# Performance work log

Measured on AMD Instinct MI355X. Metric: run time of the kernel, lower is better.

Reference implementation:

```python
import jax, jax.numpy as jnp
import numpy as np

N = 10000   # num nodes
E = 320000  # num edges (avg degree 32)
F = 128     # feat_size
H = 128     # hidden_size


def setup_inputs() -> dict:
    key = jax.random.key(0)
    ks = jax.random.split(key, 16)

    def p(k, shape, scale=0.05):
        return jax.random.normal(k, shape, jnp.float32) * scale

    inp = {
        "x": p(ks[0], (N, F), 1.0),
        "edge_index": jax.random.randint(ks[1], (2, E), 0, N),
    }
    # 6 SAGEConv layers: encoder (F->H, H->H), attr decoder (H->H, H->F),
    # struct decoder (H->H, H->N). Each has W_l (neighbor), b_l, W_r (root).
    dims = [(F, H), (H, H), (H, H), (H, F), (H, H), (H, N)]
    names = ["e1", "e2", "a1", "a2", "s1", "s2"]
    i = 2
    for name, (din, dout) in zip(names, dims):
        inp[f"Wl_{name}"] = p(ks[i], (din, dout))
        inp[f"bl_{name}"] = jnp.zeros((dout,), jnp.float32)
        inp[f"Wr_{name}"] = p(ks[i + 1], (din, dout))
        i += 2
    return inp


def sage(x, src, dst, Wl, bl, Wr, n):
    # PyG SAGEConv (aggr='mean'): mean of source-node features at each target,
    # then out = agg @ W_l + b + x @ W_r (root weight).
    msg = jax.ops.segment_sum(x[src], dst, num_segments=n)          # [n, din]
    deg = jax.ops.segment_sum(jnp.ones((src.shape[0],), x.dtype), dst, num_segments=n)
    agg = msg / jnp.maximum(deg, 1.0)[:, None]
    return agg @ Wl + bl + x @ Wr


def reference(x, edge_index,
              Wl_e1, bl_e1, Wr_e1, Wl_e2, bl_e2, Wr_e2,
              Wl_a1, bl_a1, Wr_a1, Wl_a2, bl_a2, Wr_a2,
              Wl_s1, bl_s1, Wr_s1, Wl_s2, bl_s2, Wr_s2):
    src, dst = edge_index[0], edge_index[1]
    n = x.shape[0]
    # Encoder (dropout is identity in eval mode)
    h = jax.nn.relu(sage(x, src, dst, Wl_e1, bl_e1, Wr_e1, n))
    h = jax.nn.relu(sage(h, src, dst, Wl_e2, bl_e2, Wr_e2, n))
    # Attribute decoder -> x_hat [N, F]
    xh = jax.nn.relu(sage(h, src, dst, Wl_a1, bl_a1, Wr_a1, n))
    xh = jax.nn.relu(sage(xh, src, dst, Wl_a2, bl_a2, Wr_a2, n))
    # Structure decoder -> [N, N], transposed as in the original
    s = jax.nn.relu(sage(h, src, dst, Wl_s1, bl_s1, Wr_s1, n))
    s = jax.nn.relu(sage(s, src, dst, Wl_s2, bl_s2, Wr_s2, n)).T
    return (s, xh)
```

## Files before the change

kernel.cpp:

```cpp
#include <hip/hip_runtime.h>
#include <hip/hip_bf16.h>

typedef unsigned short ushort_t;
typedef unsigned int uint_t;
typedef __attribute__((ext_vector_type(8))) short short8;
typedef __attribute__((ext_vector_type(4))) float float4v;

__device__ __forceinline__ float bf2f(ushort_t u) {
    union { uint_t i; float f; } c; c.i = ((uint_t)u) << 16; return c.f;
}
__device__ __forceinline__ ushort_t f2bf(float f) {
    union { float f; uint_t i; } c; c.f = f;
    uint_t x = c.i;
    uint_t r = x + 0x7fffu + ((x >> 16) & 1u);
    return (ushort_t)(r >> 16);
}

__device__ __forceinline__ void gl_lds16(const void* g, void* l) {
    __builtin_amdgcn_global_load_lds(
        (const __attribute__((address_space(1))) void*)g,
        (__attribute__((address_space(3))) void*)l, 16, 0, 0);
}

__device__ __forceinline__ void stv(float* p, float v) { *p = v; }
__device__ __forceinline__ void stv(ushort_t* p, float v) { *p = f2bf(v); }

__global__ void hist_kernel(const int* __restrict__ dstv, int* __restrict__ cnt, int E) {
    int e = blockIdx.x * 256 + threadIdx.x;
    if (e < E) atomicAdd(&cnt[dstv[e]], 1);
}

__global__ __launch_bounds__(1024) void scan_kernel(
    const int* __restrict__ cnt, int* __restrict__ rowptr,
    int* __restrict__ cursor, float* __restrict__ deginv, int n) {
    __shared__ int sums[1024];
    const int t = threadIdx.x;
    const int per = (n + 1023) >> 10;
    const int b0 = t * per;
    int s = 0;
    for (int u = 0; u < per; u++) {
        int i = b0 + u;
        if (i < n) s += cnt[i];
    }
    sums[t] = s;
    __syncthreads();
    int x = s;
    for (int off = 1; off < 1024; off <<= 1) {
        int y = (t >= off) ? sums[t - off] : 0;
        __syncthreads();
        x += y;
        sums[t] = x;
        __syncthreads();
    }
    int run = x - s;
    for (int u = 0; u < per; u++) {
        int i = b0 + u;
        if (i < n) {
            int v = cnt[i];
            rowptr[i] = run;
            cursor[i] = run;
            deginv[i] = 1.0f / (float)(v > 0 ? v : 1);
            run += v;
        }
    }
    if (t == 1023) rowptr[n] = x;
}

__global__ void scatter_kernel(const int* __restrict__ srcv, const int* __restrict__ dstv,
                               int* __restrict__ cursor, int* __restrict__ srcs_sorted, int E) {
    int e = blockIdx.x * 256 + threadIdx.x;
    if (e < E) {
        int p = atomicAdd(&cursor[dstv[e]], 1);
        srcs_sorted[p] = srcv[e];
    }
}

__global__ __launch_bounds__(256) void transpose_w_kernel(
    const float* __restrict__ W0, const float* __restrict__ W1,
    ushort_t* __restrict__ WT, int Nout) {
    __shared__ ushort_t tile[64][72];
    const int i0 = blockIdx.x * 64;
    const int k0 = blockIdx.y * 64;
    const float* W = (k0 < 128) ? (W0 + (size_t)k0 * Nout)
                                : (W1 + (size_t)(k0 - 128) * Nout);
    const int tid = threadIdx.x;
    const int li = tid & 63;
    const int kq = tid >> 6;
    const int gi = i0 + li;
    const bool ok = gi < Nout;
    for (int k = kq; k < 64; k += 4) {
        float v = ok ? W[(size_t)k * Nout + gi] : 0.f;
        tile[li][k] = f2bf(v);
    }
    __syncthreads();
    for (int s = tid; s < 512; s += 256) {
        int r = s >> 3, ch = s & 7;
        int gi2 = i0 + r;
        if (gi2 < Nout)
            *(short8*)(WT + (size_t)gi2 * 256 + k0 + ch * 8) = *(const short8*)&tile[r][ch * 8];
    }
}

struct W5 { const float* W0[5]; const float* W1[5]; };
__global__ __launch_bounds__(256) void transpose_w5_kernel(W5 wp, ushort_t* __restrict__ WT) {
    __shared__ ushort_t tile[64][72];
    const int layer = blockIdx.z;
    const int i0 = blockIdx.x * 64;
    const int k0 = blockIdx.y * 64;
    const float* W = (k0 < 128) ? (wp.W0[layer] + (size_t)k0 * 128)
                                : (wp.W1[layer] + (size_t)(k0 - 128) * 128);
    ushort_t* WTb = WT + (size_t)layer * 128 * 256;
    const int tid = threadIdx.x;
    const int li = tid & 63;
    const int kq = tid >> 6;
    const int gi = i0 + li;
    for (int k = kq; k < 64; k += 4)
        tile[li][k] = f2bf(W[(size_t)k * 128 + gi]);
    __syncthreads();
    for (int s = tid; s < 512; s += 256) {
        int r = s >> 3, ch = s & 7;
        *(short8*)(WTb + (size_t)(i0 + r) * 256 + k0 + ch * 8) = *(const short8*)&tile[r][ch * 8];
    }
}

template <typename TIN>
__device__ __forceinline__ float2 ld2(const TIN* act, size_t row, int t);
template <>
__device__ __forceinline__ float2 ld2<float>(const float* act, size_t row, int t) {
    return ((const float2*)act)[row * 64 + t];
}
template <>
__device__ __forceinline__ float2 ld2<ushort_t>(const ushort_t* act, size_t row, int t) {
    uint_t u = ((const uint_t*)act)[row * 64 + t];
    float2 r; r.x = bf2f((ushort_t)(u & 0xffffu)); r.y = bf2f((ushort_t)(u >> 16));
    return r;
}

template <typename TIN>
__global__ __launch_bounds__(256) void aggregate_kernel(
    const TIN* __restrict__ act, const int* __restrict__ srcs,
    const int* __restrict__ rowptr, const float* __restrict__ deginv,
    ushort_t* __restrict__ Acat, int N) {
    int node = blockIdx.x * 4 + (threadIdx.x >> 6);
    if (node >= N) return;
    int t = threadIdx.x & 63;
    int e0 = rowptr[node], e1 = rowptr[node + 1];
    float ax = 0.f, ay = 0.f;
    int e = e0;
    for (; e + 4 <= e1; e += 4) {
        int s0 = srcs[e], s1 = srcs[e + 1], s2 = srcs[e + 2], s3 = srcs[e + 3];
        float2 v0 = ld2(act, (size_t)s0, t);
        float2 v1 = ld2(act, (size_t)s1, t);
        float2 v2 = ld2(act, (size_t)s2, t);
        float2 v3 = ld2(act, (size_t)s3, t);
        ax += v0.x + v1.x + v2.x + v3.x;
        ay += v0.y + v1.y + v2.y + v3.y;
    }
    for (; e < e1; e++) {
        float2 v = ld2(act, (size_t)srcs[e], t);
        ax += v.x; ay += v.y;
    }
    float dinv = deginv[node];
    uint_t m = ((uint_t)f2bf(ay * dinv) << 16) | (uint_t)f2bf(ax * dinv);
    float2 self = ld2(act, (size_t)node, t);
    uint_t sf = ((uint_t)f2bf(self.y) << 16) | (uint_t)f2bf(self.x);
    ((uint_t*)Acat)[(size_t)node * 128 + t]      = m;
    ((uint_t*)Acat)[(size_t)node * 128 + 64 + t] = sf;
}

__global__ __launch_bounds__(256) void aggregate2_kernel(
    const ushort_t* __restrict__ act, const int* __restrict__ srcs,
    const int* __restrict__ rowptr, const float* __restrict__ deginv,
    ushort_t* __restrict__ AcatA, ushort_t* __restrict__ AcatS, int N) {
    int node = blockIdx.x * 4 + (threadIdx.x >> 6);
    if (node >= N) return;
    int t = threadIdx.x & 63;
    const uint_t* A = (const uint_t*)act;
    int e0 = rowptr[node], e1 = rowptr[node + 1];
    float ax = 0.f, ay = 0.f, sx = 0.f, sy = 0.f;
    int e = e0;
    for (; e + 2 <= e1; e += 2) {
        size_t r0 = (size_t)srcs[e] * 128, r1 = (size_t)srcs[e + 1] * 128;
        uint_t ua0 = A[r0 + t], us0 = A[r0 + 64 + t];
        uint_t ua1 = A[r1 + t], us1 = A[r1 + 64 + t];
        ax += bf2f((ushort_t)(ua0 & 0xffffu)) + bf2f((ushort_t)(ua1 & 0xffffu));
        ay += bf2f((ushort_t)(ua0 >> 16))     + bf2f((ushort_t)(ua1 >> 16));
        sx += bf2f((ushort_t)(us0 & 0xffffu)) + bf2f((ushort_t)(us1 & 0xffffu));
        sy += bf2f((ushort_t)(us0 >> 16))     + bf2f((ushort_t)(us1 >> 16));
    }
    if (e < e1) {
        size_t r0 = (size_t)srcs[e] * 128;
        uint_t ua0 = A[r0 + t], us0 = A[r0 + 64 + t];
        ax += bf2f((ushort_t)(ua0 & 0xffffu));
        ay += bf2f((ushort_t)(ua0 >> 16));
        sx += bf2f((ushort_t)(us0 & 0xffffu));
        sy += bf2f((ushort_t)(us0 >> 16));
    }
    float dinv = deginv[node];
    size_t rb = (size_t)node * 128;
    uint_t sa = A[rb + t], ss = A[rb + 64 + t];
    ((uint_t*)AcatA)[rb + t]      = ((uint_t)f2bf(ay * dinv) << 16) | (uint_t)f2bf(ax * dinv);
    ((uint_t*)AcatA)[rb + 64 + t] = sa;
    ((uint_t*)AcatS)[rb + t]      = ((uint_t)f2bf(sy * dinv) << 16) | (uint_t)f2bf(sx * dinv);
    ((uint_t*)AcatS)[rb + 64 + t] = ss;
}

template <bool BIAS_I, bool SWZ, typename TOUT>
__global__ __launch_bounds__(256) void gemm_nt_kernel(
    const ushort_t* __restrict__ A, const ushort_t* __restrict__ B,
    const float* __restrict__ bias, const float* __restrict__ bias2, int jsplit,
    TOUT* __restrict__ C, int rowsA, int rowsB, int tilesM, int tilesN) {
    __shared__ __align__(16) ushort_t Alds[128 * 64];
    __shared__ __align__(16) ushort_t Blds[128 * 64];

    int pid_m, pid_n;
    if (SWZ) {
        const int lin = blockIdx.x;
        const int nwg = gridDim.x;
        const int w = (lin & 7) * (nwg >> 3) + (lin >> 3);
        const int tM8 = (tilesM + 7) >> 3;
        const int sg = w >> 6, is = w & 63;
        const int sgm = sg % tM8, sgn = sg / tM8;
        pid_m = sgm * 8 + (is & 7);
        pid_n = sgn * 8 + (is >> 3);
        if (pid_m >= tilesM || pid_n >= tilesN) return;
    } else {
        const int lin = blockIdx.x;
        const int GRP = 8;
        const int nig = GRP * tilesN;
        const int gidg = lin / nig;
        const int first_m = gidg * GRP;
        const int gsz = min(tilesM - first_m, GRP);
        const int in_grp = lin - gidg * nig;
        pid_m = first_m + (in_grp % gsz);
        pid_n = in_grp / gsz;
    }
    const int i0 = pid_m * 128;
    const int j0 = pid_n * 128;

    const int tid  = threadIdx.x;
    const int lane = tid & 63;
    const int wid  = tid >> 6;
    const int wm = wid >> 1, wn = wid & 1;
    const int r16 = lane & 15, quad = lane >> 4;
    const int rsub = lane >> 3;
    const int csw  = (lane & 7) ^ rsub;

    float4v acc[4][4];
#pragma unroll
    for (int a = 0; a < 4; a++)
#pragma unroll
        for (int b = 0; b < 4; b++) acc[a][b] = (float4v){0.f, 0.f, 0.f, 0.f};

    for (int kt = 0; kt < 4; kt++) {
        __syncthreads();
        const int kbase = kt * 64 + csw * 8;
#pragma unroll
        for (int t = 0; t < 4; t++) {
            const int w8 = (wid * 4 + t) * 8;
            int rA = min(i0 + w8 + rsub, rowsA - 1);
            gl_lds16(A + (size_t)rA * 256 + kbase, Alds + w8 * 64);
            int rB = min(j0 + w8 + rsub, rowsB - 1);
            gl_lds16(B + (size_t)rB * 256 + kbase, Blds + w8 * 64);
        }
        __syncthreads();
#pragma unroll
        for (int ks = 0; ks < 2; ks++) {
            const int chb = ks * 4 + quad;
            const int sw = ((chb ^ (r16 & 7))) * 8;
            short8 af[4], bfr[4];
#pragma unroll
            for (int im = 0; im < 4; im++)
                af[im] = *(const short8*)(Alds + (wm * 64 + im * 16 + r16) * 64 + sw);
#pragma unroll
            for (int jn = 0; jn < 4; jn++)
                bfr[jn] = *(const short8*)(Blds + (wn * 64 + jn * 16 + r16) * 64 + sw);
#pragma unroll
            for (int im = 0; im < 4; im++)
#pragma unroll
                for (int jn = 0; jn < 4; jn++)
                    acc[im][jn] = __builtin_amdgcn_mfma_f32_16x16x32_bf16(
                        af[im], bfr[jn], acc[im][jn], 0, 0, 0);
        }
    }

    const int rows_lim = rowsA - i0;
    const int cols_lim = rowsB - j0;
#pragma unroll
    for (int im = 0; im < 4; im++) {
#pragma unroll
        for (int jn = 0; jn < 4; jn++) {
            const int jl = wn * 64 + jn * 16 + r16;
            if (jl < cols_lim) {
                float bj = 0.f;
                if (!BIAS_I) {
                    int jg = j0 + jl;
                    bj = (jg >= jsplit) ? bias2[jg - jsplit] : bias[jg];
                }
#pragma unroll
                for (int r = 0; r < 4; r++) {
                    const int il = wm * 64 + im * 16 + quad * 4 + r;
                    if (il < rows_lim) {
                        float bv = BIAS_I ? bias[i0 + il] : bj;
                        float v = fmaxf(acc[im][jn][r] + bv, 0.f);
                        stv(C + (size_t)(i0 + il) * rowsB + (j0 + jl), v);
                    }
                }
            }
        }
    }
}

extern "C" void kernel_launch(void* const* d_in, const int* in_sizes, int n_in,
                              void* d_out, int out_size, void* d_ws, size_t ws_size,
                              hipStream_t stream) {
    const int N = in_sizes[18];
    const int E = in_sizes[1] / 2;

    const float* x = (const float*)d_in[0];
    const int* ei = (const int*)d_in[1];
    const int* srcv = ei;
    const int* dstv = ei + E;

    const float* Wl[6] = {(const float*)d_in[2],  (const float*)d_in[5],
                          (const float*)d_in[8],  (const float*)d_in[11],
                          (const float*)d_in[14], (const float*)d_in[17]};
    const float* bl[6] = {(const float*)d_in[3],  (const float*)d_in[6],
                          (const float*)d_in[9],  (const float*)d_in[12],
                          (const float*)d_in[15], (const float*)d_in[18]};
    const float* Wr[6] = {(const float*)d_in[4],  (const float*)d_in[7],
                          (const float*)d_in[10], (const float*)d_in[13],
                          (const float*)d_in[16], (const float*)d_in[19]};

    char* p = (char*)d_ws;
    auto carve = [&](size_t bytes) -> char* {
        char* q = p;
        p += (bytes + 255) & ~(size_t)255;
        return q;
    };
    int*      cnt    = (int*)carve((size_t)N * 4);
    int*      rowptr = (int*)carve((size_t)(N + 1) * 4);
    int*      cursor = (int*)carve((size_t)N * 4);
    float*    deginv = (float*)carve((size_t)N * 4);
    int*      srcs   = (int*)carve((size_t)E * 4);
    ushort_t* Acat   = (ushort_t*)carve((size_t)N * 256 * 2);
    ushort_t* AcatS  = (ushort_t*)carve((size_t)N * 256 * 2);
    ushort_t* hbA    = (ushort_t*)carve((size_t)N * 128 * 2);
    ushort_t* hbB    = (ushort_t*)carve((size_t)N * 128 * 2);
    ushort_t* hbC    = (ushort_t*)carve((size_t)N * 256 * 2);
    ushort_t* WTs2   = (ushort_t*)carve((size_t)N * 256 * 2);
    ushort_t* WsT    = (ushort_t*)carve((size_t)5 * 128 * 256 * 2);

    hipMemsetAsync(cnt, 0, (size_t)N * 4, stream);
    hist_kernel<<<(E + 255) / 256, 256, 0, stream>>>(dstv, cnt, E);
    scan_kernel<<<1, 1024, 0, stream>>>(cnt, rowptr, cursor, deginv, N);
    scatter_kernel<<<(E + 255) / 256, 256, 0, stream>>>(srcv, dstv, cursor, srcs, E);

    W5 w5;
    w5.W0[0] = Wl[0]; w5.W1[0] = Wr[0];
    w5.W0[1] = Wl[1]; w5.W1[1] = Wr[1];
    w5.W0[2] = Wl[2]; w5.W1[2] = Wr[2];
    w5.W0[3] = Wl[4]; w5.W1[3] = Wr[4];
    w5.W0[4] = Wl[3]; w5.W1[4] = Wr[3];
    transpose_w5_kernel<<<dim3(2, 4, 5), 256, 0, stream>>>(w5, WsT);
    transpose_w_kernel<<<dim3((N + 63) / 64, 4), 256, 0, stream>>>(
        Wl[5], Wr[5], WTs2, N);

    float* outp = (float*)d_out;
    float* xh_out = outp + (size_t)N * N;

    const int tM = (N + 127) / 128;
    const int BIG = 1 << 30;

    aggregate_kernel<float><<<(N + 3) / 4, 256, 0, stream>>>(x, srcs, rowptr, deginv, Acat, N);
    gemm_nt_kernel<false, false, ushort_t><<<tM, 256, 0, stream>>>(
        Acat, WsT + 0 * 128 * 256, bl[0], nullptr, BIG, hbA, N, 128, tM, 1);
    aggregate_kernel<ushort_t><<<(N + 3) / 4, 256, 0, stream>>>(hbA, srcs, rowptr, deginv, Acat, N);
    gemm_nt_kernel<false, false, ushort_t><<<tM, 256, 0, stream>>>(
        Acat, WsT + 1 * 128 * 256, bl[1], nullptr, BIG, hbB, N, 128, tM, 1);
    aggregate_kernel<ushort_t><<<(N + 3) / 4, 256, 0, stream>>>(hbB, srcs, rowptr, deginv, Acat, N);
    gemm_nt_kernel<false, false, ushort_t><<<tM * 2, 256, 0, stream>>>(
        Acat, WsT + 2 * 128 * 256, bl[2], bl[4], 128, hbC, N, 256, tM, 2);
    aggregate2_kernel<<<(N + 3) / 4, 256, 0, stream>>>(hbC, srcs, rowptr, deginv, Acat, AcatS, N);
    gemm_nt_kernel<false, false, float><<<tM, 256, 0, stream>>>(
        Acat, WsT + 4 * 128 * 256, bl[3], nullptr, BIG, xh_out, N, 128, tM, 1);
    const int tM8 = (tM + 7) / 8;
    gemm_nt_kernel<true, true, float><<<tM8 * tM8 * 64, 256, 0, stream>>>(
        WTs2, AcatS, bl[5], nullptr, BIG, outp, N, N, tM, tM);

    (void)n_in; (void)out_size; (void)ws_size;
}
```

Baseline: 750.2 us.

## Stage fp32 GEMM epilogue through LDS for coalesced stores; 64-row tiles for small GEMMs

The fp32 output epilogue now writes each 32-row chunk of the accumulator tile into shared memory and then stores it back as row-contiguous float4 writes. This targets the big N×N structure output, whose per-lane scalar stores were strided. The small 128-wide GEMMs switch to 64-row M tiles to launch more workgroups, and the dual aggregation loop is unrolled by four edges to keep more gathers in flight. The LDS staging adds extra syncthreads per chunk and reuses the operand buffers.

```diff
diff --git a/kernel.cpp b/kernel.cpp
--- a/kernel.cpp
+++ b/kernel.cpp
@@ -179,16 +179,23 @@
     int e0 = rowptr[node], e1 = rowptr[node + 1];
     float ax = 0.f, ay = 0.f, sx = 0.f, sy = 0.f;
     int e = e0;
-    for (; e + 2 <= e1; e += 2) {
-        size_t r0 = (size_t)srcs[e] * 128, r1 = (size_t)srcs[e + 1] * 128;
+    for (; e + 4 <= e1; e += 4) {
+        size_t r0 = (size_t)srcs[e] * 128,     r1 = (size_t)srcs[e + 1] * 128;
+        size_t r2 = (size_t)srcs[e + 2] * 128, r3 = (size_t)srcs[e + 3] * 128;
         uint_t ua0 = A[r0 + t], us0 = A[r0 + 64 + t];
         uint_t ua1 = A[r1 + t], us1 = A[r1 + 64 + t];
-        ax += bf2f((ushort_t)(ua0 & 0xffffu)) + bf2f((ushort_t)(ua1 & 0xffffu));
-        ay += bf2f((ushort_t)(ua0 >> 16))     + bf2f((ushort_t)(ua1 >> 16));
-        sx += bf2f((ushort_t)(us0 & 0xffffu)) + bf2f((ushort_t)(us1 & 0xffffu));
-        sy += bf2f((ushort_t)(us0 >> 16))     + bf2f((ushort_t)(us1 >> 16));
-    }
-    if (e < e1) {
+        uint_t ua2 = A[r2 + t], us2 = A[r2 + 64 + t];
+        uint_t ua3 = A[r3 + t], us3 = A[r3 + 64 + t];
+        ax += bf2f((ushort_t)(ua0 & 0xffffu)) + bf2f((ushort_t)(ua1 & 0xffffu))
+            + bf2f((ushort_t)(ua2 & 0xffffu)) + bf2f((ushort_t)(ua3 & 0xffffu));
+        ay += bf2f((ushort_t)(ua0 >> 16))     + bf2f((ushort_t)(ua1 >> 16))
+            + bf2f((ushort_t)(ua2 >> 16))     + bf2f((ushort_t)(ua3 >> 16));
+        sx += bf2f((ushort_t)(us0 & 0xffffu)) + bf2f((ushort_t)(us1 & 0xffffu))
+            + bf2f((ushort_t)(us2 & 0xffffu)) + bf2f((ushort_t)(us3 & 0xffffu));
+        sy += bf2f((ushort_t)(us0 >> 16))     + bf2f((ushort_t)(us1 >> 16))
+            + bf2f((ushort_t)(us2 >> 16))     + bf2f((ushort_t)(us3 >> 16));
+    }
+    for (; e < e1; e++) {
         size_t r0 = (size_t)srcs[e] * 128;
         uint_t ua0 = A[r0 + t], us0 = A[r0 + 64 + t];
         ax += bf2f((ushort_t)(ua0 & 0xffffu));
@@ -205,13 +212,15 @@
     ((uint_t*)AcatS)[rb + 64 + t] = ss;
 }
 
-template <bool BIAS_I, bool SWZ, typename TOUT>
+template <bool BIAS_I, bool SWZ, int TM, typename TOUT>
 __global__ __launch_bounds__(256) void gemm_nt_kernel(
     const ushort_t* __restrict__ A, const ushort_t* __restrict__ B,
     const float* __restrict__ bias, const float* __restrict__ bias2, int jsplit,
     TOUT* __restrict__ C, int rowsA, int rowsB, int tilesM, int tilesN) {
-    __shared__ __align__(16) ushort_t Alds[128 * 64];
-    __shared__ __align__(16) ushort_t Blds[128 * 64];
+    constexpr int IMN = TM / 32;
+    __shared__ __align__(16) char smem[TM * 128 + 16384];
+    ushort_t* Alds = (ushort_t*)smem;
+    ushort_t* Blds = (ushort_t*)(smem + TM * 128);
 
     int pid_m, pid_n;
     if (SWZ) {
@@ -235,7 +244,7 @@
         pid_m = first_m + (in_grp % gsz);
         pid_n = in_grp / gsz;
     }
-    const int i0 = pid_m * 128;
+    const int i0 = pid_m * TM;
     const int j0 = pid_n * 128;
 
     const int tid  = threadIdx.x;
@@ -246,9 +255,9 @@
     const int rsub = lane >> 3;
     const int csw  = (lane & 7) ^ rsub;
 
-    float4v acc[4][4];
-#pragma unroll
-    for (int a = 0; a < 4; a++)
+    float4v acc[IMN][4];
+#pragma unroll
+    for (int a = 0; a < IMN; a++)
 #pragma unroll
         for (int b = 0; b < 4; b++) acc[a][b] = (float4v){0.f, 0.f, 0.f, 0.f};
 
@@ -256,10 +265,14 @@
         __syncthreads();
         const int kbase = kt * 64 + csw * 8;
 #pragma unroll
+        for (int t = 0; t < IMN; t++) {
+            const int w8 = (wid * IMN + t) * 8;
+            int rA = min(i0 + w8 + rsub, rowsA - 1);
+            gl_lds16(A + (size_t)rA * 256 + kbase, Alds + w8 * 64);
+        }
+#pragma unroll
         for (int t = 0; t < 4; t++) {
             const int w8 = (wid * 4 + t) * 8;
-            int rA = min(i0 + w8 + rsub, rowsA - 1);
-            gl_lds16(A + (size_t)rA * 256 + kbase, Alds + w8 * 64);
             int rB = min(j0 + w8 + rsub, rowsB - 1);
             gl_lds16(B + (size_t)rB * 256 + kbase, Blds + w8 * 64);
         }
@@ -268,15 +281,15 @@
         for (int ks = 0; ks < 2; ks++) {
             const int chb = ks * 4 + quad;
             const int sw = ((chb ^ (r16 & 7))) * 8;
-            short8 af[4], bfr[4];
-#pragma unroll
-            for (int im = 0; im < 4; im++)
-                af[im] = *(const short8*)(Alds + (wm * 64 + im * 16 + r16) * 64 + sw);
+            short8 af[IMN], bfr[4];
+#pragma unroll
+            for (int im = 0; im < IMN; im++)
+                af[im] = *(const short8*)(Alds + (wm * (TM / 2) + im * 16 + r16) * 64 + sw);
 #pragma unroll
             for (int jn = 0; jn < 4; jn++)
                 bfr[jn] = *(const short8*)(Blds + (wn * 64 + jn * 16 + r16) * 64 + sw);
 #pragma unroll
-            for (int im = 0; im < 4; im++)
+            for (int im = 0; im < IMN; im++)
 #pragma unroll
                 for (int jn = 0; jn < 4; jn++)
                     acc[im][jn] = __builtin_amdgcn_mfma_f32_16x16x32_bf16(
@@ -286,24 +299,74 @@
 
     const int rows_lim = rowsA - i0;
     const int cols_lim = rowsB - j0;
-#pragma unroll
-    for (int im = 0; im < 4; im++) {
-#pragma unroll
-        for (int jn = 0; jn < 4; jn++) {
-            const int jl = wn * 64 + jn * 16 + r16;
-            if (jl < cols_lim) {
-                float bj = 0.f;
-                if (!BIAS_I) {
-                    int jg = j0 + jl;
-                    bj = (jg >= jsplit) ? bias2[jg - jsplit] : bias[jg];
+
+    if constexpr (sizeof(TOUT) == 4) {
+        float* T = (float*)smem;
+        constexpr int NCH = TM / 32;
+#pragma unroll
+        for (int c = 0; c < NCH; c++) {
+            const int crow = c * 32;
+            __syncthreads();
+            if (wm == crow / (TM / 2)) {
+                const int imb = (crow - wm * (TM / 2)) / 16;
+#pragma unroll
+                for (int ii = 0; ii < 2; ii++) {
+                    const int im = imb + ii;
+#pragma unroll
+                    for (int jn = 0; jn < 4; jn++) {
+                        const int jl = wn * 64 + jn * 16 + r16;
+                        float bj = 0.f;
+                        if (!BIAS_I) {
+                            int jg = j0 + jl;
+                            bj = (jg >= jsplit) ? bias2[jg - jsplit] : bias[jg];
+                        }
+#pragma unroll
+                        for (int r = 0; r < 4; r++) {
+                            const int rl = ii * 16 + quad * 4 + r;
+                            float bv = BIAS_I ? bias[min(i0 + crow + rl, rowsA - 1)] : bj;
+                            T[rl * 132 + jl] = fmaxf(acc[im][jn][r] + bv, 0.f);
+                        }
+                    }
                 }
-#pragma unroll
-                for (int r = 0; r < 4; r++) {
-                    const int il = wm * 64 + im * 16 + quad * 4 + r;
-                    if (il < rows_lim) {
-                        float bv = BIAS_I ? bias[i0 + il] : bj;
-                        float v = fmaxf(acc[im][jn][r] + bv, 0.f);
-                        stv(C + (size_t)(i0 + il) * rowsB + (j0 + jl), v);
+            }
+            __syncthreads();
+            const int c4 = tid & 31, rl0 = tid >> 5;
+#pragma unroll
+            for (int s = 0; s < 4; s++) {
+                const int rl = rl0 + s * 8;
+                const int il = crow + rl;
+                if (il < rows_lim) {
+                    const int jl = c4 * 4;
+                    float* dst = (float*)C + (size_t)(i0 + il) * rowsB + j0 + jl;
+                    if (jl + 4 <= cols_lim) {
+                        *(float4v*)dst = *(const float4v*)&T[rl * 132 + jl];
+                    } else {
+                        for (int jj = 0; jj < 4; jj++)
+                            if (jl + jj < cols_lim) dst[jj] = T[rl * 132 + jl + jj];
+                    }
+                }
+            }
+        }
+    } else {
+#pragma unroll
+        for (int im = 0; im < IMN; im++) {
+#pragma unroll
+            for (int jn = 0; jn < 4; jn++) {
+                const int jl = wn * 64 + jn * 16 + r16;
+                if (jl < cols_lim) {
+                    float bj = 0.f;
+                    if (!BIAS_I) {
+                        int jg = j0 + jl;
+                        bj = (jg >= jsplit) ? bias2[jg - jsplit] : bias[jg];
+                    }
+#pragma unroll
+                    for (int r = 0; r < 4; r++) {
+                        const int il = wm * (TM / 2) + im * 16 + quad * 4 + r;
+                        if (il < rows_lim) {
+                            float bv = BIAS_I ? bias[i0 + il] : bj;
+                            float v = fmaxf(acc[im][jn][r] + bv, 0.f);
+                            stv(C + (size_t)(i0 + il) * rowsB + (j0 + jl), v);
+                        }
                     }
                 }
             }
@@ -369,24 +432,25 @@
     float* outp = (float*)d_out;
     float* xh_out = outp + (size_t)N * N;
 
-    const int tM = (N + 127) / 128;
+    const int tM128 = (N + 127) / 128;
+    const int tM64  = (N + 63) / 64;
     const int BIG = 1 << 30;
 
     aggregate_kernel<float><<<(N + 3) / 4, 256, 0, stream>>>(x, srcs, rowptr, deginv, Acat, N);
-    gemm_nt_kernel<false, false, ushort_t><<<tM, 256, 0, stream>>>(
-        Acat, WsT + 0 * 128 * 256, bl[0], nullptr, BIG, hbA, N, 128, tM, 1);
+    gemm_nt_kernel<false, false, 64, ushort_t><<<tM64, 256, 0, stream>>>(
+        Acat, WsT + 0 * 128 * 256, bl[0], nullptr, BIG, hbA, N, 128, tM64, 1);
     aggregate_kernel<ushort_t><<<(N + 3) / 4, 256, 0, stream>>>(hbA, srcs, rowptr, deginv, Acat, N);
-    gemm_nt_kernel<false, false, ushort_t><<<tM, 256, 0, stream>>>(
-        Acat, WsT + 1 * 128 * 256, bl[1], nullptr, BIG, hbB, N, 128, tM, 1);
+    gemm_nt_kernel<false, false, 64, ushort_t><<<tM64, 256, 0, stream>>>(
+        Acat, WsT + 1 * 128 * 256, bl[1], nullptr, BIG, hbB, N, 128, tM64, 1);
     aggregate_kernel<ushort_t><<<(N + 3) / 4, 256, 0, stream>>>(hbB, srcs, rowptr, deginv, Acat, N);
-    gemm_nt_kernel<false, false, ushort_t><<<tM * 2, 256, 0, stream>>>(
-        Acat, WsT + 2 * 128 * 256, bl[2], bl[4], 128, hbC, N, 256, tM, 2);
+    gemm_nt_kernel<false, false, 64, ushort_t><<<tM64 * 2, 256, 0, stream>>>(
+        Acat, WsT + 2 * 128 * 256, bl[2], bl[4], 128, hbC, N, 256, tM64, 2);
     aggregate2_kernel<<<(N + 3) / 4, 256, 0, stream>>>(hbC, srcs, rowptr, deginv, Acat, AcatS, N);
-    gemm_nt_kernel<false, false, float><<<tM, 256, 0, stream>>>(
-        Acat, WsT + 4 * 128 * 256, bl[3], nullptr, BIG, xh_out, N, 128, tM, 1);
-    const int tM8 = (tM + 7) / 8;
-    gemm_nt_kernel<true, true, float><<<tM8 * tM8 * 64, 256, 0, stream>>>(
-        WTs2, AcatS, bl[5], nullptr, BIG, outp, N, N, tM, tM);
+    gemm_nt_kernel<false, false, 64, float><<<tM64, 256, 0, stream>>>(
+        Acat, WsT + 4 * 128 * 256, bl[3], nullptr, BIG, xh_out, N, 128, tM64, 1);
+    const int tM8 = (tM128 + 7) / 8;
+    gemm_nt_kernel<true, true, 128, float><<<tM8 * tM8 * 64, 256, 0, stream>>>(
+        WTs2, AcatS, bl[5], nullptr, BIG, outp, N, N, tM128, tM128);
 
     (void)n_in; (void)out_size; (void)ws_size;
 }
```

Measured after the change: 673.9 us. -10.2%, faster.
